# Kernel optimization log

Measured on AMD Instinct MI355X. Metric: run time of the kernel, lower is better.

The kernel has to match this reference:

```python
import jax, jax.numpy as jnp
import numpy as np

PS, PAD, STRIDE = 3, 1, 1  # patch_size, padding, strides


def _unfold(x, ps, pad, stride):
    # torch F.unfold: [N, C, H, W] -> [N, C*ps*ps, L], channel-major (c, i, j) ordering
    N, C, H, Wd = x.shape
    xp = jnp.pad(x, ((0, 0), (0, 0), (pad, pad), (pad, pad)))
    Ho = (H + 2 * pad - ps) // stride + 1
    Wo = (Wd + 2 * pad - ps) // stride + 1
    cols = [xp[:, :, i:i + stride * Ho:stride, j:j + stride * Wo:stride]
            for i in range(ps) for j in range(ps)]  # ps*ps tensors of [N, C, Ho, Wo]
    cols = jnp.stack(cols, axis=2)                  # [N, C, ps*ps, Ho, Wo]
    return cols.reshape(N, C * ps * ps, Ho * Wo)


def _fold(cols, out_hw, ps, pad, stride):
    # torch F.fold (scatter-add inverse of unfold)
    N, CPP, L = cols.shape
    C = CPP // (ps * ps)
    H, Wd = out_hw
    Ho = (H + 2 * pad - ps) // stride + 1
    Wo = (Wd + 2 * pad - ps) // stride + 1
    cols = cols.reshape(N, C, ps, ps, Ho, Wo)
    out = jnp.zeros((N, C, H + 2 * pad, Wd + 2 * pad), cols.dtype)
    for i in range(ps):
        for j in range(ps):
            out = out.at[:, :, i:i + stride * Ho:stride, j:j + stride * Wo:stride].add(cols[:, :, i, j])
    return out[:, :, pad:pad + H, pad:pad + Wd]


def _l2norm(x, eps=1e-12):
    n = jnp.sqrt(jnp.sum(x * x, axis=-1, keepdims=True))
    return x / jnp.maximum(n, eps)


def setup_inputs() -> dict:
    key = jax.random.key(0)
    k1, k2, k3, k4 = jax.random.split(key, 4)
    shp = (2, 64, 5, 5, 48, 48)  # b, c, ah, aw, h, w
    return {
        "x1": jax.random.normal(k1, shp, dtype=jnp.float32),
        "x2": jax.random.normal(k2, shp, dtype=jnp.float32),
        "x3": jax.random.normal(k3, shp, dtype=jnp.float32),
        "W": jax.random.normal(k4, (8, 64), dtype=jnp.float32) * 0.05,  # 1x1 conv, c -> c//8
    }


def reference(x1, x2, x3, W):
    b, c, ah, aw, h, w = x1.shape
    A = ah * aw

    def flat(x):  # b c ah aw h w -> (b ah aw) c h w
        return x.transpose(0, 2, 3, 1, 4, 5).reshape(b * A, c, h, w)

    q = jnp.einsum('oc,nchw->nohw', W, flat(x1))  # 1x1 conv, no bias
    k = jnp.einsum('oc,nchw->nohw', W, flat(x2))
    v = flat(x3)

    qc = _unfold(q, PS, PAD, STRIDE)  # [(b ah aw), p_q, L]
    kc = _unfold(k, PS, PAD, STRIDE)
    vc = _unfold(v, PS, PAD, STRIDE)  # [(b ah aw), p_v, L]
    L = vc.shape[-1]
    p_v = vc.shape[1]

    def re(t):  # (b ah aw) p n -> b n (ah aw p)
        p = t.shape[1]
        return t.reshape(b, A, p, L).transpose(0, 3, 1, 2).reshape(b, L, A * p)

    Q = _l2norm(re(qc))
    K = _l2norm(re(kc))
    V = re(vc)  # [b, L, A*p_v]

    attn = jnp.einsum('bnd,bmd->bnm', Q, K)       # [b, L, L] cosine similarity
    idx = jnp.argmax(attn, axis=-1)               # [b, L] hard attention
    out = jnp.take_along_axis(V, idx[:, :, None], axis=1)  # gather rows of V

    # b n (ah aw p) -> (b ah aw) p n
    out = out.reshape(b, L, A, p_v).transpose(0, 2, 3, 1).reshape(b * A, p_v, L)
    out = _fold(out, (h, w), PS, PAD, STRIDE)     # [(b ah aw), c, h, w]
    return out.reshape(b, ah, aw, c, h, w).transpose(0, 3, 1, 2, 4, 5)
```

## Files before the change

kernel.cpp:

```cpp
#include <hip/hip_runtime.h>
#include <math.h>
#include <float.h>

#define NPIX 2304
#define NPAD 2500
#define PLANE 573440
#define MARGIN 3e-4f

#define OFF_QP     0u
#define OFF_KP     1146880u
#define OFF_PLANES 2293760u
#define OFF_NK     4587520u
#define OFF_INVNK  4592520u
#define OFF_PVAL   4597128u
#define OFF_PSEC   4818312u
#define OFF_PIDX   5039496u
#define OFF_IDX    5260680u
#define OFF_FLAG   5265288u
#define OFF_S      5269896u
#define OFF_SOFF   OFF_S
#define SSTRIDE    6250000L
#define PLANE_SH   573440

typedef __attribute__((ext_vector_type(8))) short short8;
typedef __attribute__((ext_vector_type(4))) float f32x4;

__device__ __forceinline__ unsigned short bfhi(float f) {
    unsigned u = __float_as_uint(f);
    return (unsigned short)((u + 0x7FFFu + ((u >> 16) & 1u)) >> 16);
}

__device__ __forceinline__ void gload_lds16(const void* g, void* l) {
    __builtin_amdgcn_global_load_lds(
        (const __attribute__((address_space(1))) unsigned int*)g,
        (__attribute__((address_space(3))) unsigned int*)l, 16, 0, 0);
}

__global__ __launch_bounds__(256) void k_zero(float4* __restrict__ p, int n4) {
    int i = blockIdx.x * 256 + threadIdx.x;
    const int stride = gridDim.x * 256;
    const float4 z = { 0.f, 0.f, 0.f, 0.f };
    for (; i < n4; i += stride) p[i] = z;
}

__global__ __launch_bounds__(256) void k_qk(const float* __restrict__ x1,
                                            const float* __restrict__ x2,
                                            const float* __restrict__ W,
                                            float* __restrict__ qp,
                                            float* __restrict__ kp,
                                            unsigned short* __restrict__ planes) {
    __shared__ float Ws[512];
    const int t = threadIdx.x;
    Ws[t] = W[t];
    Ws[t + 256] = W[t + 256];
    __syncthreads();
    const int img = blockIdx.x / 9;
    const int chunk = blockIdx.x % 9;
    const int pix = chunk * 256 + t;
    const int b = img / 25, a = img % 25;
    const int y = pix / 48, x = pix % 48;

    float q[8], k[8];
#pragma unroll
    for (int o = 0; o < 8; ++o) { q[o] = 0.f; k[o] = 0.f; }

    const float* p1 = x1 + (size_t)b * 64 * 57600 + a * 2304 + pix;
    const float* p2 = x2 + (size_t)b * 64 * 57600 + a * 2304 + pix;
    for (int c = 0; c < 64; ++c) {
        float v1 = p1[c * 57600];
        float v2 = p2[c * 57600];
#pragma unroll
        for (int o = 0; o < 8; ++o) {
            float w = Ws[o * 64 + c];
            q[o] = fmaf(w, v1, q[o]);
            k[o] = fmaf(w, v2, k[o]);
        }
    }
    const int p = (y + 1) * 50 + (x + 1);
    float* qd = qp + (size_t)b * PLANE + (size_t)p * 224 + a * 8;
    float* kd = kp + (size_t)b * PLANE + (size_t)p * 224 + a * 8;
    float4 q0 = { q[0], q[1], q[2], q[3] }, q1 = { q[4], q[5], q[6], q[7] };
    float4 k0 = { k[0], k[1], k[2], k[3] }, k1 = { k[4], k[5], k[6], k[7] };
    *(float4*)qd = q0; *(float4*)(qd + 4) = q1;
    *(float4*)kd = k0; *(float4*)(kd + 4) = k1;

    const int P = p >> 7, r = p & 127, cc = a >> 2, dq = a & 3;
    const int g = r * 4 + ((dq + (r >> 1)) & 3);
    const size_t goff = ((size_t)(P * 7 + cc) * 512 + g) * 8;
    short8 qh, ql, kh, kl;
#pragma unroll
    for (int o = 0; o < 8; ++o) {
        unsigned short h = bfhi(q[o]);
        qh[o] = (short)h;
        ql[o] = (short)bfhi(q[o] - __uint_as_float(((unsigned)h) << 16));
        h = bfhi(k[o]);
        kh[o] = (short)h;
        kl[o] = (short)bfhi(k[o] - __uint_as_float(((unsigned)h) << 16));
    }
    *(short8*)(planes + (size_t)(0 * 2 + b) * PLANE_SH + goff) = qh;
    *(short8*)(planes + (size_t)(1 * 2 + b) * PLANE_SH + goff) = ql;
    *(short8*)(planes + (size_t)(2 * 2 + b) * PLANE_SH + goff) = kh;
    *(short8*)(planes + (size_t)(3 * 2 + b) * PLANE_SH + goff) = kl;
}

__global__ void k_nk(const float* __restrict__ kp, float* __restrict__ nk) {
    int t = blockIdx.x * 256 + threadIdx.x;
    if (t >= 2 * NPAD) return;
    int b = t / NPAD, p = t - b * NPAD;
    const float* src = kp + (size_t)b * PLANE + (size_t)p * 224;
    float s = 0.f;
    for (int d = 0; d < 200; d += 4) {
        float4 v = *(const float4*)(src + d);
        s = fmaf(v.x, v.x, s); s = fmaf(v.y, v.y, s);
        s = fmaf(v.z, v.z, s); s = fmaf(v.w, v.w, s);
    }
    nk[t] = s;
}

__global__ void k_invnk(const float* __restrict__ nk, float* __restrict__ invNk) {
    int t = blockIdx.x * 256 + threadIdx.x;
    if (t >= 2 * NPIX) return;
    int b = t / NPIX, m = t - b * NPIX;
    int my = m / 48, mx = m % 48;
    const float* nb = nk + b * NPAD;
    float s = 0.f;
#pragma unroll
    for (int i = 0; i < 3; ++i)
#pragma unroll
        for (int j = 0; j < 3; ++j)
            s += nb[(my + i) * 50 + mx + j];
    invNk[t] = 1.0f / fmaxf(sqrtf(s), 1e-12f);
}

__global__ __launch_bounds__(256, 2) void k_mfma2(const unsigned short* __restrict__ planes,
                                                  float* __restrict__ S,
                                                  long sStride, int bofs) {
    __shared__ unsigned short Abuf[2][4096];
    __shared__ unsigned short Bbuf[2][4096];
    const int t = threadIdx.x;
    const int nwg = gridDim.x * gridDim.y * gridDim.z;
    const int lin = (blockIdx.z * gridDim.y + blockIdx.y) * gridDim.x + blockIdx.x;
    const int work = (lin & 7) * (nwg >> 3) + (lin >> 3);
    const int z = work / 400;
    const int rem = work - z * 400;
    const int wy = rem / 20, wx = rem - (rem / 20) * 20;
    const int b = bofs + z;

    const unsigned short* Ahi = planes + (size_t)(0 * 2 + b) * PLANE_SH;
    const unsigned short* Alo = planes + (size_t)(1 * 2 + b) * PLANE_SH;
    const unsigned short* Bhi = planes + (size_t)(2 * 2 + b) * PLANE_SH;
    const unsigned short* Blo = planes + (size_t)(3 * 2 + b) * PLANE_SH;
    float* Sb = S + (size_t)z * sStride;

    const int p0 = wy * 128, r0 = wx * 128;
    const int wid = t >> 6, l = t & 63;
    const int lp = l & 15, dq = l >> 4;
    const int wqp = (wid >> 1) * 64, wqr = (wid & 1) * 64;

    int aoff[4], boff[4];
#pragma unroll
    for (int tr = 0; tr < 4; ++tr) {
        int rA = wqp + tr * 16 + lp;
        aoff[tr] = (rA * 4 + ((dq + (rA >> 1)) & 3)) * 8;
        int rB = wqr + tr * 16 + lp;
        boff[tr] = (rB * 4 + ((dq + (rB >> 1)) & 3)) * 8;
    }

    f32x4 acc[4][4];
#pragma unroll
    for (int i = 0; i < 4; ++i)
#pragma unroll
        for (int j = 0; j < 4; ++j) acc[i][j] = (f32x4){0.f, 0.f, 0.f, 0.f};

#define STAGE(buf, ks)                                                          \
    {                                                                           \
        const int term = (ks) / 7, c = (ks) - term * 7;                         \
        const unsigned short* gA = (term < 2 ? Ahi : Alo) + ((size_t)(wy * 7 + c) << 12); \
        const unsigned short* gB = (term != 1 ? Bhi : Blo) + ((size_t)(wx * 7 + c) << 12); \
        unsigned short* lA = &Abuf[buf][wid * 512];                             \
        unsigned short* lB = &Bbuf[buf][wid * 512];                             \
        gload_lds16(gA + t * 8, lA);                                            \
        gload_lds16(gA + 2048 + t * 8, lA + 2048);                              \
        gload_lds16(gB + t * 8, lB);                                            \
        gload_lds16(gB + 2048 + t * 8, lB + 2048);                              \
    }

    STAGE(0, 0);
    asm volatile("s_waitcnt vmcnt(0)" ::: "memory");
    __syncthreads();

    int cur = 0;
    for (int ks = 0; ks < 21; ++ks) {
        if (ks + 1 < 21) STAGE(cur ^ 1, ks + 1);
        {
            const unsigned short* Ab = &Abuf[cur][0];
            const unsigned short* Bb = &Bbuf[cur][0];
            short8 af[4], bfr[4];
#pragma unroll
            for (int tr = 0; tr < 4; ++tr) af[tr] = *(const short8*)(Ab + aoff[tr]);
#pragma unroll
            for (int tc = 0; tc < 4; ++tc) bfr[tc] = *(const short8*)(Bb + boff[tc]);
#pragma unroll
            for (int tr = 0; tr < 4; ++tr)
#pragma unroll
                for (int tc = 0; tc < 4; ++tc)
                    acc[tr][tc] = __builtin_amdgcn_mfma_f32_16x16x32_bf16(
                        af[tr], bfr[tc], acc[tr][tc], 0, 0, 0);
        }
        if (ks + 1 < 21) {
            asm volatile("s_waitcnt vmcnt(0)" ::: "memory");
            __syncthreads();
            cur ^= 1;
        }
    }
#undef STAGE

#pragma unroll
    for (int tr = 0; tr < 4; ++tr) {
#pragma unroll
        for (int v = 0; v < 4; ++v) {
            const int p = p0 + wqp + tr * 16 + dq * 4 + v;
            if (p < NPAD) {
                float* srow_ = Sb + (size_t)p * NPAD;
#pragma unroll
                for (int tc = 0; tc < 4; ++tc) {
                    const int c = r0 + wqr + tc * 16 + lp;
                    if (c < NPAD) srow_[c] = acc[tr][tc][v];
                }
            }
        }
    }
}

__global__ __launch_bounds__(384) void k_argmax(const float* __restrict__ S,
                                                const float* __restrict__ invNk,
                                                float* __restrict__ pval,
                                                float* __restrict__ psec,
                                                int* __restrict__ pidx,
                                                long sStride, int bofs) {
    __shared__ float band[3][50][50];
    const int t = threadIdx.x;
    const int my = blockIdx.x;
    const int ly = blockIdx.y;
    const int batch = bofs + blockIdx.z;
    const float* Sb = S + (size_t)blockIdx.z * sStride;

    {
        const int rt = t >> 3, ct = t & 7;
        for (int rr = rt; rr < 150; rr += 48) {
            const int i = (rr >= 100) ? 2 : (rr >= 50 ? 1 : 0);
            const int uu = rr - i * 50;
            const float* srow = Sb + (size_t)((ly + i) * 50 + uu) * NPAD + (my + i) * 50;
            float* drow = &band[i][uu][0];
            *(float2*)(drow + 2 * ct)      = *(const float2*)(srow + 2 * ct);
            *(float2*)(drow + 16 + 2 * ct) = *(const float2*)(srow + 16 + 2 * ct);
            *(float2*)(drow + 32 + 2 * ct) = *(const float2*)(srow + 32 + 2 * ct);
            if (ct == 0) *(float2*)(drow + 48) = *(const float2*)(srow + 48);
        }
    }
    __syncthreads();

    const int lx = t >> 3;
    const int mc = t & 7;
    const float* inb = invNk + batch * NPIX;
    const float* bp = &band[0][lx][mc];

    float b1 = -FLT_MAX, b2 = -FLT_MAX;
    int i1 = 0x7FFFFFFF;

#pragma unroll
    for (int k = 0; k < 6; ++k) {
        const float* p = bp + 8 * k;
        float s = p[0]    + p[51]   + p[102]
                + p[2500] + p[2551] + p[2602]
                + p[5000] + p[5051] + p[5102];
        int m = my * 48 + mc + (k << 3);
        float v = s * inb[m];
        if (v > b1 || (v == b1 && m < i1)) { b2 = b1; b1 = v; i1 = m; }
        else b2 = fmaxf(b2, v);
    }
#pragma unroll
    for (int off = 1; off < 8; off <<= 1) {
        float ob1 = __shfl_xor(b1, off, 64);
        int oi1 = __shfl_xor(i1, off, 64);
        float ob2 = __shfl_xor(b2, off, 64);
        if (ob1 > b1 || (ob1 == b1 && oi1 < i1)) { b2 = fmaxf(b1, ob2); b1 = ob1; i1 = oi1; }
        else b2 = fmaxf(b2, ob1);
    }
    if (mc == 0) {
        int o = (batch * 48 + my) * NPIX + ly * 48 + lx;
        pval[o] = b1;
        psec[o] = b2;
        pidx[o] = i1;
    }
}

__global__ void k_argred(const float* __restrict__ pval, const float* __restrict__ psec,
                         const int* __restrict__ pidx, int* __restrict__ idxout,
                         int* __restrict__ flag) {
    int t = blockIdx.x * 256 + threadIdx.x;
    if (t >= 2 * NPIX) return;
    int b = t / NPIX, lcl = t - b * NPIX;
    float b1 = -FLT_MAX, b2 = -FLT_MAX;
    int i1 = 0x7FFFFFFF;
    for (int my = 0; my < 48; ++my) {
        int o = (b * 48 + my) * NPIX + lcl;
        float v1 = pval[o], v2 = psec[o];
        int ii = pidx[o];
        if (v1 > b1 || (v1 == b1 && ii < i1)) { b2 = fmaxf(b1, v2); b1 = v1; i1 = ii; }
        else b2 = fmaxf(b2, v1);
    }
    idxout[t] = i1;
    flag[t] = (b1 - b2 < MARGIN) ? 1 : 0;
}

__global__ __launch_bounds__(256) void k_fix2(const float* __restrict__ qp,
                                              const float* __restrict__ kp,
                                              const float* __restrict__ S,
                                              const float* __restrict__ invNk,
                                              const float* __restrict__ pval,
                                              const float* __restrict__ psec,
                                              const int* __restrict__ pidx,
                                              const int* __restrict__ flag,
                                              int* __restrict__ idx,
                                              long sStride, int bofs) {
    const int t = threadIdx.x;
    const int lane = t & 63;
    const int row = blockIdx.x * 4 + (t >> 6);
    const int z = blockIdx.y;
    const int b = bofs + z;
    if (!flag[b * NPIX + row]) return;
    const float* Sb = S + (size_t)z * sStride;
    const float* Ap = qp + (size_t)b * PLANE;
    const float* Bp = kp + (size_t)b * PLANE;
    const float* inb = invNk + b * NPIX;
    const int ly = row / 48, lx = row % 48;

    float v1 = -FLT_MAX, v2 = -FLT_MAX;
    if (lane < 48) {
        int o = (b * 48 + lane) * NPIX + row;
        v1 = pval[o];
        v2 = psec[o];
    }
    float bb = v1;
#pragma unroll
    for (int off = 1; off < 64; off <<= 1)
        bb = fmaxf(bb, __shfl_xor(bb, off, 64));
    const float th = bb - MARGIN;

    unsigned long long mask = __ballot(lane < 48 && (v1 >= th || v2 >= th));
    float eb = -FLT_MAX;
    int ebi = 0x7FFFFFFF;
    while (mask) {
        const int my = __ffsll((long long)mask) - 1;
        mask &= mask - 1;
        float va = -FLT_MAX;
        if (lane < 48) {
            float s = 0.f;
#pragma unroll
            for (int i = 0; i < 3; ++i)
#pragma unroll
                for (int j = 0; j < 3; ++j)
                    s += Sb[(size_t)((ly + i) * 50 + lx + j) * NPAD + (my + i) * 50 + lane + j];
            va = s * inb[my * 48 + lane];
        }
        unsigned long long m2 = __ballot(lane < 48 && va >= th);
        while (m2) {
            const int mx = __ffsll((long long)m2) - 1;
            m2 &= m2 - 1;
            const int m = my * 48 + mx;
            float part = 0.f;
#pragma unroll
            for (int ij = 0; ij < 9; ++ij) {
                const float* qr = Ap + (size_t)((ly + ij / 3) * 50 + lx + ij % 3) * 224;
                const float* kr = Bp + (size_t)((my + ij / 3) * 50 + mx + ij % 3) * 224;
                for (int d = lane; d < 200; d += 64)
                    part = fmaf(qr[d], kr[d], part);
            }
#pragma unroll
            for (int off = 1; off < 64; off <<= 1)
                part += __shfl_xor(part, off, 64);
            const float v = part * inb[m];
            if (v > eb) { eb = v; ebi = m; }
        }
    }
    if (lane == 0 && ebi != 0x7FFFFFFF) idx[b * NPIX + row] = ebi;
}

__global__ void k_soff(const int* __restrict__ idx, int* __restrict__ soff) {
    int t = blockIdx.x * 256 + threadIdx.x;
    if (t >= 2 * NPIX) return;
    int b = t / NPIX, pix = t - b * NPIX;
    int y = pix / 48, x = pix % 48;
#pragma unroll
    for (int i = 0; i < 3; ++i) {
#pragma unroll
        for (int j = 0; j < 3; ++j) {
            int u = i * 3 + j;
            int yq = y + 1 - i, xq = x + 1 - j;
            int so = -1;
            if (yq >= 0 && yq < 48 && xq >= 0 && xq < 48) {
                int m = idx[b * NPIX + yq * 48 + xq];
                int my = m / 48, mx = m % 48;
                int yy = my + i - 1, xx = mx + j - 1;
                if (yy >= 0 && yy < 48 && xx >= 0 && xx < 48) so = yy * 48 + xx;
            }
            soff[(b * 9 + u) * NPIX + pix] = so;
        }
    }
}

#define CPB 4
__global__ __launch_bounds__(256) void k_out2(const float* __restrict__ x3,
                                              const int* __restrict__ soff,
                                              float* __restrict__ out) {
    __shared__ __align__(16) float plane[NPIX];
    const int t = threadIdx.x;
    const int img = blockIdx.x;
    const int b = img / 25, a = img % 25;

    int po[9][9];
#pragma unroll
    for (int u = 0; u < 9; ++u) {
        const int* sb = soff + (b * 9 + u) * NPIX;
#pragma unroll
        for (int k = 0; k < 9; ++k)
            po[k][u] = sb[k * 256 + t];
    }

    const size_t pbase = (size_t)b * 64 * 57600 + (size_t)a * 2304 +
                         (size_t)(blockIdx.y * CPB) * 57600;
    const float* gsrc = x3 + pbase;
    float* gdst = out + pbase;

    float4 r0, r1, r2;
    {
        const float4* g = (const float4*)gsrc;
        r0 = g[t]; r1 = g[t + 256];
        if (t < 64) r2 = g[t + 512];
    }
    float4* pl4 = (float4*)plane;
    pl4[t] = r0; pl4[t + 256] = r1;
    if (t < 64) pl4[t + 512] = r2;
    __syncthreads();

    for (int c = 0; c < CPB; ++c) {
        if (c + 1 < CPB) {
            const float4* g = (const float4*)(gsrc + (size_t)(c + 1) * 57600);
            r0 = g[t]; r1 = g[t + 256];
            if (t < 64) r2 = g[t + 512];
        }
        float* dst = gdst + (size_t)c * 57600;
#pragma unroll
        for (int k = 0; k < 9; ++k) {
            float acc = 0.f;
#pragma unroll
            for (int u = 0; u < 9; ++u) {
                int off = po[k][u];
                int ao = off < 0 ? 0 : off;
                float v = plane[ao];
                acc += (off < 0) ? 0.f : v;
            }
            dst[k * 256 + t] = acc;
        }
        __syncthreads();
        if (c + 1 < CPB) {
            pl4[t] = r0; pl4[t + 256] = r1;
            if (t < 64) pl4[t + 512] = r2;
        }
        __syncthreads();
    }
}

extern "C" void kernel_launch(void* const* d_in, const int* in_sizes, int n_in,
                              void* d_out, int out_size, void* d_ws, size_t ws_size,
                              hipStream_t stream) {
    const float* x1 = (const float*)d_in[0];
    const float* x2 = (const float*)d_in[1];
    const float* x3 = (const float*)d_in[2];
    const float* W  = (const float*)d_in[3];
    float* ws = (float*)d_ws;

    float* qp    = ws + OFF_QP;
    float* kp    = ws + OFF_KP;
    unsigned short* planes = (unsigned short*)(ws + OFF_PLANES);
    float* nk    = ws + OFF_NK;
    float* invNk = ws + OFF_INVNK;
    float* pval  = ws + OFF_PVAL;
    float* psec  = ws + OFF_PSEC;
    int*   pidx  = (int*)(ws + OFF_PIDX);
    int*   idx   = (int*)(ws + OFF_IDX);
    int*   flag  = (int*)(ws + OFF_FLAG);
    float* S     = ws + OFF_S;
    int*   soff  = (int*)(ws + OFF_SOFF);
    float* out   = (float*)d_out;

    const bool bigS = ws_size >= (size_t)(OFF_S + 2UL * (unsigned long)SSTRIDE) * 4UL;

    k_zero<<<2048, 256, 0, stream>>>((float4*)(ws + OFF_QP), (int)(OFF_NK / 4));

    k_qk<<<450, 256, 0, stream>>>(x1, x2, W, qp, kp, planes);
    k_nk<<<(2 * NPAD + 255) / 256, 256, 0, stream>>>(kp, nk);
    k_invnk<<<(2 * NPIX + 255) / 256, 256, 0, stream>>>(nk, invNk);

    if (bigS) {
        k_mfma2<<<dim3(20, 20, 2), 256, 0, stream>>>(planes, S, SSTRIDE, 0);
        k_argmax<<<dim3(48, 48, 2), 384, 0, stream>>>(S, invNk, pval, psec, pidx, SSTRIDE, 0);
        k_argred<<<18, 256, 0, stream>>>(pval, psec, pidx, idx, flag);
        k_fix2<<<dim3(576, 2), 256, 0, stream>>>(qp, kp, S, invNk, pval, psec, pidx,
                                                 flag, idx, SSTRIDE, 0);
    } else {
        for (int b = 0; b < 2; ++b) {
            k_mfma2<<<dim3(20, 20, 1), 256, 0, stream>>>(planes, S, 0L, b);
            k_argmax<<<dim3(48, 48, 1), 384, 0, stream>>>(S, invNk, pval, psec, pidx, 0L, b);
            k_argred<<<18, 256, 0, stream>>>(pval, psec, pidx, idx, flag);
            k_fix2<<<dim3(576, 1), 256, 0, stream>>>(qp, kp, S, invNk, pval, psec,
                                                     pidx, flag, idx, 0L, b);
        }
    }
    k_soff<<<(2 * NPIX + 255) / 256, 256, 0, stream>>>(idx, soff);
    k_out2<<<dim3(50, 16), 256, 0, stream>>>(x3, soff, out);
}
```

Before: 179.7 us.

## Fuse argmax reduction into fix kernel and swizzle argmax block order

```diff
diff --git a/kernel.cpp b/kernel.cpp
--- a/kernel.cpp
+++ b/kernel.cpp
@@ -16,7 +16,6 @@
 #define OFF_PSEC   4818312u
 #define OFF_PIDX   5039496u
 #define OFF_IDX    5260680u
-#define OFF_FLAG   5265288u
 #define OFF_S      5269896u
 #define OFF_SOFF   OFF_S
 #define SSTRIDE    6250000L
@@ -66,6 +65,7 @@
 
     const float* p1 = x1 + (size_t)b * 64 * 57600 + a * 2304 + pix;
     const float* p2 = x2 + (size_t)b * 64 * 57600 + a * 2304 + pix;
+#pragma unroll 8
     for (int c = 0; c < 64; ++c) {
         float v1 = p1[c * 57600];
         float v2 = p2[c * 57600];
@@ -240,10 +240,15 @@
                                                 long sStride, int bofs) {
     __shared__ float band[3][50][50];
     const int t = threadIdx.x;
-    const int my = blockIdx.x;
-    const int ly = blockIdx.y;
-    const int batch = bofs + blockIdx.z;
-    const float* Sb = S + (size_t)blockIdx.z * sStride;
+    const int nwg = gridDim.x * gridDim.y * gridDim.z;
+    const int lin = (blockIdx.z * gridDim.y + blockIdx.y) * gridDim.x + blockIdx.x;
+    const int work = (lin & 7) * (nwg >> 3) + (lin >> 3);
+    const int z = work / 2304;
+    const int w2 = work - z * 2304;
+    const int ly = w2 / 48;
+    const int my = w2 - ly * 48;
+    const int batch = bofs + z;
+    const float* Sb = S + (size_t)z * sStride;
 
     {
         const int rt = t >> 3, ct = t & 7;
@@ -295,58 +300,48 @@
     }
 }
 
-__global__ void k_argred(const float* __restrict__ pval, const float* __restrict__ psec,
-                         const int* __restrict__ pidx, int* __restrict__ idxout,
-                         int* __restrict__ flag) {
-    int t = blockIdx.x * 256 + threadIdx.x;
-    if (t >= 2 * NPIX) return;
-    int b = t / NPIX, lcl = t - b * NPIX;
-    float b1 = -FLT_MAX, b2 = -FLT_MAX;
-    int i1 = 0x7FFFFFFF;
-    for (int my = 0; my < 48; ++my) {
-        int o = (b * 48 + my) * NPIX + lcl;
-        float v1 = pval[o], v2 = psec[o];
-        int ii = pidx[o];
-        if (v1 > b1 || (v1 == b1 && ii < i1)) { b2 = fmaxf(b1, v2); b1 = v1; i1 = ii; }
-        else b2 = fmaxf(b2, v1);
-    }
-    idxout[t] = i1;
-    flag[t] = (b1 - b2 < MARGIN) ? 1 : 0;
-}
-
-__global__ __launch_bounds__(256) void k_fix2(const float* __restrict__ qp,
-                                              const float* __restrict__ kp,
-                                              const float* __restrict__ S,
-                                              const float* __restrict__ invNk,
-                                              const float* __restrict__ pval,
-                                              const float* __restrict__ psec,
-                                              const int* __restrict__ pidx,
-                                              const int* __restrict__ flag,
-                                              int* __restrict__ idx,
-                                              long sStride, int bofs) {
+__global__ __launch_bounds__(256) void k_sel(const float* __restrict__ qp,
+                                             const float* __restrict__ kp,
+                                             const float* __restrict__ S,
+                                             const float* __restrict__ invNk,
+                                             const float* __restrict__ pval,
+                                             const float* __restrict__ psec,
+                                             const int* __restrict__ pidx,
+                                             int* __restrict__ idx,
+                                             long sStride, int bofs) {
     const int t = threadIdx.x;
     const int lane = t & 63;
     const int row = blockIdx.x * 4 + (t >> 6);
     const int z = blockIdx.y;
     const int b = bofs + z;
-    if (!flag[b * NPIX + row]) return;
+
+    float v1 = -FLT_MAX, v2 = -FLT_MAX;
+    int ii = 0x7FFFFFFF;
+    if (lane < 48) {
+        int o = (b * 48 + lane) * NPIX + row;
+        v1 = pval[o];
+        v2 = psec[o];
+        ii = pidx[o];
+    }
+    float r1 = v1, r2 = v2;
+    int ri = ii;
+#pragma unroll
+    for (int off = 1; off < 64; off <<= 1) {
+        float o1 = __shfl_xor(r1, off, 64);
+        int oi = __shfl_xor(ri, off, 64);
+        float o2 = __shfl_xor(r2, off, 64);
+        if (o1 > r1 || (o1 == r1 && oi < ri)) { r2 = fmaxf(o2, r1); r1 = o1; ri = oi; }
+        else r2 = fmaxf(r2, o1);
+    }
+    if (lane == 0) idx[b * NPIX + row] = ri;
+    if (r1 - r2 >= MARGIN) return;
+
     const float* Sb = S + (size_t)z * sStride;
     const float* Ap = qp + (size_t)b * PLANE;
     const float* Bp = kp + (size_t)b * PLANE;
     const float* inb = invNk + b * NPIX;
     const int ly = row / 48, lx = row % 48;
-
-    float v1 = -FLT_MAX, v2 = -FLT_MAX;
-    if (lane < 48) {
-        int o = (b * 48 + lane) * NPIX + row;
-        v1 = pval[o];
-        v2 = psec[o];
-    }
-    float bb = v1;
-#pragma unroll
-    for (int off = 1; off < 64; off <<= 1)
-        bb = fmaxf(bb, __shfl_xor(bb, off, 64));
-    const float th = bb - MARGIN;
+    const float th = r1 - MARGIN;
 
     unsigned long long mask = __ballot(lane < 48 && (v1 >= th || v2 >= th));
     float eb = -FLT_MAX;
@@ -490,7 +485,6 @@
     float* psec  = ws + OFF_PSEC;
     int*   pidx  = (int*)(ws + OFF_PIDX);
     int*   idx   = (int*)(ws + OFF_IDX);
-    int*   flag  = (int*)(ws + OFF_FLAG);
     float* S     = ws + OFF_S;
     int*   soff  = (int*)(ws + OFF_SOFF);
     float* out   = (float*)d_out;
@@ -506,16 +500,14 @@
     if (bigS) {
         k_mfma2<<<dim3(20, 20, 2), 256, 0, stream>>>(planes, S, SSTRIDE, 0);
         k_argmax<<<dim3(48, 48, 2), 384, 0, stream>>>(S, invNk, pval, psec, pidx, SSTRIDE, 0);
-        k_argred<<<18, 256, 0, stream>>>(pval, psec, pidx, idx, flag);
-        k_fix2<<<dim3(576, 2), 256, 0, stream>>>(qp, kp, S, invNk, pval, psec, pidx,
-                                                 flag, idx, SSTRIDE, 0);
+        k_sel<<<dim3(576, 2), 256, 0, stream>>>(qp, kp, S, invNk, pval, psec, pidx,
+                                                idx, SSTRIDE, 0);
     } else {
         for (int b = 0; b < 2; ++b) {
             k_mfma2<<<dim3(20, 20, 1), 256, 0, stream>>>(planes, S, 0L, b);
             k_argmax<<<dim3(48, 48, 1), 384, 0, stream>>>(S, invNk, pval, psec, pidx, 0L, b);
-            k_argred<<<18, 256, 0, stream>>>(pval, psec, pidx, idx, flag);
-            k_fix2<<<dim3(576, 1), 256, 0, stream>>>(qp, kp, S, invNk, pval, psec,
-                                                     pidx, flag, idx, 0L, b);
+            k_sel<<<dim3(576, 1), 256, 0, stream>>>(qp, kp, S, invNk, pval, psec, pidx,
+                                                    idx, 0L, b);
         }
     }
     k_soff<<<(2 * NPIX + 255) / 256, 256, 0, stream>>>(idx, soff);
```

After: 147.5 us. 17.9% less time.
